# Optimization experiments

Hardware: AMD Instinct MI355X
Metric: run time of the kernel (lower is better)

Reference implementation:

```python
import jax, jax.numpy as jnp
import numpy as np

B, D, H, L = 65536, 512, 1024, 64
LOG2PI = float(np.log(2.0 * np.pi))


def setup_inputs() -> dict:
    key = jax.random.key(0)
    ks = jax.random.split(key, 16)
    s = jnp.float32(0.02)

    def w(k, shape):
        return jax.random.normal(k, shape, dtype=jnp.float32) * s

    return {
        "x": jax.random.normal(ks[0], (B, D), dtype=jnp.float32),
        "eps": jax.random.normal(ks[1], (B, L), dtype=jnp.float32),
        # encoder params (Linear stored as [in, out] for x @ W + b)
        "W_enc_h": w(ks[2], (D, H)), "b_enc_h": jnp.zeros((H,), jnp.float32),
        "W_enc_mu": w(ks[3], (H, L)), "b_enc_mu": jnp.zeros((L,), jnp.float32),
        "W_enc_lv": w(ks[4], (H, L)), "b_enc_lv": jnp.zeros((L,), jnp.float32),
        # decoder params
        "W_dec_h": w(ks[5], (L, H)), "b_dec_h": jnp.zeros((H,), jnp.float32),
        "W_dec_mu": w(ks[6], (H, D)), "b_dec_mu": jnp.zeros((D,), jnp.float32),
        "W_dec_lv": w(ks[7], (H, D)), "b_dec_lv": jnp.zeros((D,), jnp.float32),
    }


def reference(x, eps, W_enc_h, b_enc_h, W_enc_mu, b_enc_mu, W_enc_lv, b_enc_lv,
              W_dec_h, b_dec_h, W_dec_mu, b_dec_mu, W_dec_lv, b_dec_lv):
    beta = jnp.float32(1.0)
    # encoder
    h = jnp.tanh(x @ W_enc_h + b_enc_h)                      # [B, H]
    mu_z = h @ W_enc_mu + b_enc_mu                           # [B, L]
    lv_z = h @ W_enc_lv + b_enc_lv                           # [B, L]
    # reparameterised sample
    z = mu_z + jnp.exp(0.5 * lv_z) * eps                     # [B, L]
    # decoder
    hd = jnp.tanh(z @ W_dec_h + b_dec_h)                     # [B, H]
    mu_x = jax.nn.softmax(hd @ W_dec_mu + b_dec_mu, axis=-1) # [B, D]
    lv_x = hd @ W_dec_lv + b_dec_lv                          # [B, D]
    # KL(q(z|x) || N(0, I))
    kl = -0.5 * jnp.sum(1.0 + lv_z - mu_z ** 2 - jnp.exp(lv_z), axis=-1)  # [B]
    # diagonal Gaussian log-likelihood (closed form of MultivariateNormal
    # with diag_embed(exp(ln_var)) covariance)
    ln_pxz = -0.5 * jnp.sum(lv_x + (x - mu_x) ** 2 * jnp.exp(-lv_x) + LOG2PI, axis=-1)  # [B]
    return jnp.mean(ln_pxz - beta * kl)
```

## Files before the change

kernel.cpp:

```cpp
#include <hip/hip_runtime.h>

typedef unsigned char u8;
typedef unsigned short u16;
typedef unsigned int u32;
typedef long i64;
typedef __attribute__((ext_vector_type(2))) long long2v;
typedef __attribute__((ext_vector_type(4))) float floatx4;

#define LOG2PI_F 1.8378770664093453f

__device__ __forceinline__ u16 f2bf(float f) {
  union { float f; u32 i; } c; c.f = f;
  u32 i = c.i;
  u32 r = (i + 0x7fffu + ((i >> 16) & 1u)) >> 16;
  return (u16)r;
}
__device__ __forceinline__ float bf2f(u16 u) {
  union { u32 i; float f; } c; c.i = ((u32)u) << 16; return c.f;
}
__device__ __forceinline__ u8 f2fp8(float f) {
  int p = __builtin_amdgcn_cvt_pk_fp8_f32(f, f, 0, false);
  return (u8)(p & 0xff);
}
__device__ __forceinline__ u32 pk4fp8(float a, float b, float c, float d) {
  int lo = __builtin_amdgcn_cvt_pk_fp8_f32(a, b, 0, false);
  int v  = __builtin_amdgcn_cvt_pk_fp8_f32(c, d, lo, true);
  return (u32)v;
}
__device__ __forceinline__ float fast_tanh(float x) {
  float xc = fminf(fmaxf(x, -10.f), 10.f);
  float t = __expf(2.f * xc);
  return (t - 1.f) * __builtin_amdgcn_rcpf(t + 1.f);
}
__device__ __forceinline__ void llds16(const void* g, void* l) {
  __builtin_amdgcn_global_load_lds(
      (const __attribute__((address_space(1))) u32*)g,
      (__attribute__((address_space(3))) u32*)l, 16, 0, 0);
}
__device__ __forceinline__ u32 permk(u32 k) {
  u32 g = k & ~63u, o = (k >> 3) & 7u, r = k & 7u;
  u32 po = ((o & 3u) << 1) | (o >> 2);
  return g | (po << 3) | r;
}

#define INV_4096  2.44140625e-4f
#define INV_16384 6.103515625e-5f

__global__ void pack_xb(const float* __restrict__ in, u32* __restrict__ out, int n4) {
  int i = blockIdx.x * 256 + threadIdx.x;
  if (i >= n4) return;
  const float4 v = ((const float4*)in)[i];
  int row = i >> 7;
  int k = (i & 127) << 2;
  int kp = permk(k);
  out[(row << 7) + (kp >> 2)] = pk4fp8(v.x * 16.f, v.y * 16.f, v.z * 16.f, v.w * 16.f);
}

__global__ void pack_wt(const float* __restrict__ W, u8* __restrict__ Wt, int K, int N) {
  int idx = blockIdx.x * 256 + threadIdx.x;
  if (idx >= K * N) return;
  int k = idx / N, n = idx - k * N;
  Wt[(size_t)n * K + permk(k)] = f2fp8(W[idx] * 256.f);
}

__global__ void pack_wt2(const float* __restrict__ W1, const float* __restrict__ W2,
                         u8* __restrict__ Wt, int K, int N1, int N2) {
  int idx = blockIdx.x * 256 + threadIdx.x;
  if (idx >= (N1 + N2) * K) return;
  int n = idx / K, k = idx - n * K;
  float v = (n < N1) ? W1[(size_t)k * N1 + n] : W2[(size_t)k * N2 + (n - N1)];
  Wt[(size_t)n * K + permk(k)] = f2fp8(v * 256.f);
}

__global__ void catf(const float* __restrict__ a, const float* __restrict__ b,
                     float* __restrict__ o, int n1, int n2) {
  int i = blockIdx.x * 256 + threadIdx.x;
  if (i < n1) o[i] = a[i];
  else if (i < n1 + n2) o[i] = b[i - n1];
}

__global__ __launch_bounds__(256) void gemm_bt0(
    const u8* __restrict__ A, const u8* __restrict__ Bt,
    const float* __restrict__ bias, u8* __restrict__ C,
    float inv, float outs, int M, int N, int K) {
  __shared__ __align__(16) u8 smem[16384];
  u8* As = smem;
  u8* Bs = smem + 8192;
  const int t = threadIdx.x;
  const int wave = t >> 6, lane = t & 63;
  const int quad = lane >> 4, l16 = lane & 15;
  const int bm = blockIdx.y * 128, bn = blockIdx.x * 128;
  const int wm = (wave >> 1) * 64, wn = (wave & 1) * 64;

  floatx4 acc[4][4];
#pragma unroll
  for (int i = 0; i < 4; ++i)
#pragma unroll
    for (int j = 0; j < 4; ++j) acc[i][j] = (floatx4){0.f, 0.f, 0.f, 0.f};

  for (int kt = 0; kt < K; kt += 64) {
#pragma unroll
    for (int i = 0; i < 2; ++i) {
      int c = i * 256 + t;
      int r = c >> 2, kcS = c & 3;
      int kc = kcS ^ ((r >> 1) & 3);
      llds16(A + (size_t)(bm + r) * K + kt + kc * 16, &As[c * 16]);
      llds16(Bt + (size_t)(bn + r) * K + kt + kc * 16, &Bs[c * 16]);
    }
    __builtin_amdgcn_s_waitcnt(0);
    __syncthreads();

    long2v a2[4], b2[4];
#pragma unroll
    for (int mi = 0; mi < 4; ++mi) {
      int m = wm + mi * 16 + l16;
      a2[mi] = *(const long2v*)&As[(4 * m + (quad ^ ((m >> 1) & 3))) * 16];
    }
#pragma unroll
    for (int ni = 0; ni < 4; ++ni) {
      int n = wn + ni * 16 + l16;
      b2[ni] = *(const long2v*)&Bs[(4 * n + (quad ^ ((n >> 1) & 3))) * 16];
    }
#pragma unroll
    for (int h = 0; h < 2; ++h)
#pragma unroll
      for (int mi = 0; mi < 4; ++mi)
#pragma unroll
        for (int ni = 0; ni < 4; ++ni)
          acc[mi][ni] = __builtin_amdgcn_mfma_f32_16x16x32_fp8_fp8(
              a2[mi][h], b2[ni][h], acc[mi][ni], 0, 0, 0);
    __syncthreads();
  }

#pragma unroll
  for (int ni = 0; ni < 4; ++ni) {
    int col = wn + ni * 16 + l16;
    float bv = bias[bn + col];
    u32 pc = permk((u32)col);
#pragma unroll
    for (int mi = 0; mi < 4; ++mi) {
#pragma unroll
      for (int r = 0; r < 4; ++r) {
        int row = wm + mi * 16 + quad * 4 + r;
        float v = acc[mi][ni][r] * inv + bv;
        smem[row * 128 + pc] = f2fp8(fast_tanh(v) * outs);
      }
    }
  }
  __syncthreads();
#pragma unroll
  for (int j = 0; j < 4; ++j) {
    int u = j * 256 + t;
    int row = u >> 3, c16 = u & 7;
    *(long2v*)(C + (size_t)(bm + row) * N + bn + c16 * 16) =
        *(const long2v*)&smem[row * 128 + c16 * 16];
  }
}

template <int EPI>
__global__ __launch_bounds__(512, 2) void gemm256(
    const u8* __restrict__ A, const u8* __restrict__ Bt,
    const float* __restrict__ bias, void* __restrict__ Cv,
    float inv, float outs, int M, int N, int K) {
  __shared__ __align__(16) u8 lds[4][2][256 * 64];
  const int t = threadIdx.x;
  const int wave = t >> 6, lane = t & 63;
  const int quad = lane >> 4, l16 = lane & 15;
  const int nbx = N >> 8;
  const int nwg = nbx * (M >> 8);
  int raw = blockIdx.x + nbx * blockIdx.y;
  int wgid = ((nwg & 7) == 0) ? ((raw & 7) * (nwg >> 3) + (raw >> 3)) : raw;
  const int bm = (wgid / nbx) << 8, bn = (wgid % nbx) << 8;
  const int wm = (wave >> 2) * 128, wn = (wave & 3) * 64;
  const int nt = K >> 6;

  auto stage = [&](int ti) {
    const int b = ti & 3;
    const int kt = ti << 6;
#pragma unroll
    for (int i = 0; i < 2; ++i) {
      int c = i * 512 + t;
      int r = c >> 2, kcS = c & 3;
      int kc = kcS ^ ((r >> 1) & 3);
      llds16(A + (size_t)(bm + r) * K + kt + kc * 16, &lds[b][0][c * 16]);
    }
#pragma unroll
    for (int i = 0; i < 2; ++i) {
      int c = i * 512 + t;
      int r = c >> 2, kcS = c & 3;
      int kc = kcS ^ ((r >> 1) & 3);
      llds16(Bt + (size_t)(bn + r) * K + kt + kc * 16, &lds[b][1][c * 16]);
    }
  };

  int offA[8], offB[4];
#pragma unroll
  for (int mi = 0; mi < 8; ++mi) {
    int m = wm + mi * 16 + l16;
    offA[mi] = (4 * m + (quad ^ ((m >> 1) & 3))) * 16;
  }
#pragma unroll
  for (int ni = 0; ni < 4; ++ni) {
    int n = wn + ni * 16 + l16;
    offB[ni] = (4 * n + (quad ^ ((n >> 1) & 3))) * 16;
  }

  floatx4 acc[8][4];
#pragma unroll
  for (int i = 0; i < 8; ++i)
#pragma unroll
    for (int j = 0; j < 4; ++j) acc[i][j] = (floatx4){0.f, 0.f, 0.f, 0.f};

  long2v a2[8], b2[4], b3[4];

  stage(0);
  stage(1);
  asm volatile("s_waitcnt vmcnt(4)" ::: "memory");
  __builtin_amdgcn_s_barrier();
  asm volatile("" ::: "memory");
  {
    const u8* bA = &lds[0][0][0];
    const u8* bB = &lds[0][1][0];
#pragma unroll
    for (int ni = 0; ni < 4; ++ni) b2[ni] = *(const long2v*)(bB + offB[ni]);
#pragma unroll
    for (int mi = 0; mi < 8; ++mi) a2[mi] = *(const long2v*)(bA + offA[mi]);
  }

#define GBODY(TI, BCUR, BNXT) {                                               \
    const int ti_ = (TI);                                                     \
    if (ti_ + 2 < nt) {                                                       \
      stage(ti_ + 2);                                                         \
      asm volatile("s_waitcnt vmcnt(4)" ::: "memory");                        \
    } else {                                                                  \
      asm volatile("s_waitcnt vmcnt(0)" ::: "memory");                        \
    }                                                                         \
    __builtin_amdgcn_s_barrier();                                             \
    asm volatile("" ::: "memory");                                            \
    const u8* bA_ = &lds[(ti_ + 1) & 3][0][0];                                \
    const u8* bB_ = &lds[(ti_ + 1) & 3][1][0];                                \
    _Pragma("unroll")                                                         \
    for (int ni = 0; ni < 4; ++ni) BNXT[ni] = *(const long2v*)(bB_ + offB[ni]);\
    __builtin_amdgcn_s_setprio(1);                                            \
    _Pragma("unroll")                                                         \
    for (int mi = 0; mi < 8; ++mi) {                                          \
      _Pragma("unroll")                                                       \
      for (int h = 0; h < 2; ++h)                                             \
        _Pragma("unroll")                                                     \
        for (int ni = 0; ni < 4; ++ni)                                        \
          acc[mi][ni] = __builtin_amdgcn_mfma_f32_16x16x32_fp8_fp8(           \
              a2[mi][h], BCUR[ni][h], acc[mi][ni], 0, 0, 0);                  \
      a2[mi] = *(const long2v*)(bA_ + offA[mi]);                              \
    }                                                                         \
    __builtin_amdgcn_s_setprio(0);                                            \
  }

  int ti = 0;
  for (; ti + 2 < nt; ti += 2) {
    GBODY(ti, b2, b3);
    GBODY(ti + 1, b3, b2);
  }
  GBODY(ti, b2, b3);
#undef GBODY
  __builtin_amdgcn_s_setprio(1);
#pragma unroll
  for (int mi = 0; mi < 8; ++mi)
#pragma unroll
    for (int h = 0; h < 2; ++h)
#pragma unroll
      for (int ni = 0; ni < 4; ++ni)
        acc[mi][ni] = __builtin_amdgcn_mfma_f32_16x16x32_fp8_fp8(
            a2[mi][h], b3[ni][h], acc[mi][ni], 0, 0, 0);
  __builtin_amdgcn_s_setprio(0);

  __syncthreads();
  u8* eb = &lds[0][0][0];
  if (EPI == 0) {
#pragma unroll
    for (int ni = 0; ni < 4; ++ni) {
      int col = wn + ni * 16 + l16;
      float bv = bias[bn + col];
      u32 pc = permk((u32)col);
#pragma unroll
      for (int mi = 0; mi < 8; ++mi) {
#pragma unroll
        for (int r = 0; r < 4; ++r) {
          int row = wm + mi * 16 + quad * 4 + r;
          float v = acc[mi][ni][r] * inv + bv;
          eb[row * 256 + pc] = f2fp8(fast_tanh(v) * outs);
        }
      }
    }
    __syncthreads();
#pragma unroll
    for (int j = 0; j < 8; ++j) {
      int u = j * 512 + t;
      int row = u >> 4, c16 = u & 15;
      *(long2v*)((u8*)Cv + (size_t)(bm + row) * N + bn + c16 * 16) =
          *(const long2v*)&eb[row * 256 + c16 * 16];
    }
  } else {
    u16* ebw = (u16*)eb;
#pragma unroll
    for (int ni = 0; ni < 4; ++ni) {
      int col = wn + ni * 16 + l16;
      float bv = bias[bn + col];
#pragma unroll
      for (int mi = 0; mi < 8; ++mi) {
#pragma unroll
        for (int r = 0; r < 4; ++r) {
          int row = wm + mi * 16 + quad * 4 + r;
          float v = acc[mi][ni][r] * inv + bv;
          ebw[row * 256 + col] = f2bf(v);
        }
      }
    }
    __syncthreads();
#pragma unroll
    for (int j = 0; j < 16; ++j) {
      int u = j * 512 + t;
      int row = u >> 5, c16 = u & 31;
      *(long2v*)((u16*)Cv + (size_t)(bm + row) * N + bn + c16 * 8) =
          *(const long2v*)&ebw[row * 256 + c16 * 8];
    }
  }
}

__global__ __launch_bounds__(256) void gemm_z(
    const u8* __restrict__ A, const u8* __restrict__ Bt,
    const float* __restrict__ bias, const float* __restrict__ eps,
    u8* __restrict__ z, float* __restrict__ accp, int M, int K) {
  __shared__ __align__(16) u8 As[128 * 64];
  __shared__ __align__(16) u8 Bs[128 * 64];
  __shared__ float sexp[128 * 64];
  const int t = threadIdx.x;
  const int wave = t >> 6, lane = t & 63;
  const int quad = lane >> 4, l16 = lane & 15;
  const int bm = blockIdx.y * 128;
  const int wm = (wave >> 1) * 64, wn = (wave & 1) * 64;

  floatx4 acc[4][4];
#pragma unroll
  for (int i = 0; i < 4; ++i)
#pragma unroll
    for (int j = 0; j < 4; ++j) acc[i][j] = (floatx4){0.f, 0.f, 0.f, 0.f};

  for (int kt = 0; kt < K; kt += 64) {
#pragma unroll
    for (int i = 0; i < 2; ++i) {
      int c = i * 256 + t;
      int r = c >> 2, kcS = c & 3;
      int kc = kcS ^ ((r >> 1) & 3);
      llds16(A + (size_t)(bm + r) * K + kt + kc * 16, &As[c * 16]);
      llds16(Bt + (size_t)r * K + kt + kc * 16, &Bs[c * 16]);
    }
    __builtin_amdgcn_s_waitcnt(0);
    __syncthreads();

    long2v a2[4], b2[4];
#pragma unroll
    for (int mi = 0; mi < 4; ++mi) {
      int m = wm + mi * 16 + l16;
      a2[mi] = *(const long2v*)&As[(4 * m + (quad ^ ((m >> 1) & 3))) * 16];
    }
#pragma unroll
    for (int ni = 0; ni < 4; ++ni) {
      int n = wn + ni * 16 + l16;
      b2[ni] = *(const long2v*)&Bs[(4 * n + (quad ^ ((n >> 1) & 3))) * 16];
    }
#pragma unroll
    for (int h = 0; h < 2; ++h)
#pragma unroll
      for (int mi = 0; mi < 4; ++mi)
#pragma unroll
        for (int ni = 0; ni < 4; ++ni)
          acc[mi][ni] = __builtin_amdgcn_mfma_f32_16x16x32_fp8_fp8(
              a2[mi][h], b2[ni][h], acc[mi][ni], 0, 0, 0);
    __syncthreads();
  }

  const bool is_lv = (wave & 1);
  float kl = 0.f;
#pragma unroll
  for (int ni = 0; ni < 4; ++ni) {
    int col = wn + ni * 16 + l16;
    float bv = bias[col];
#pragma unroll
    for (int mi = 0; mi < 4; ++mi) {
#pragma unroll
      for (int r = 0; r < 4; ++r) {
        int row = wm + mi * 16 + quad * 4 + r;
        float v = acc[mi][ni][r] * INV_16384 + bv;
        if (is_lv) {
          kl += 1.0f + v - __expf(v);
          sexp[row * 64 + (col - 64)] = __expf(0.5f * v);
        } else {
          kl -= v * v;
        }
      }
    }
  }
  __syncthreads();
  if (!is_lv) {
#pragma unroll
    for (int ni = 0; ni < 4; ++ni) {
      int col = wn + ni * 16 + l16;
      float bv = bias[col];
#pragma unroll
      for (int mi = 0; mi < 4; ++mi) {
#pragma unroll
        for (int r = 0; r < 4; ++r) {
          int row = wm + mi * 16 + quad * 4 + r;
          float mu = acc[mi][ni][r] * INV_16384 + bv;
          size_t grow = (size_t)(bm + row);
          float ep = eps[grow * 64 + col];
          z[grow * 64 + permk(col)] = f2fp8((mu + sexp[row * 64 + col] * ep) * 16.f);
        }
      }
    }
  }
  kl *= 0.5f;
  for (int off = 32; off > 0; off >>= 1) kl += __shfl_xor(kl, off, 64);
  __shared__ float s4[4];
  if (lane == 0) s4[wave] = kl;
  __syncthreads();
  if (t == 0) atomicAdd(accp, s4[0] + s4[1] + s4[2] + s4[3]);
}

__global__ __launch_bounds__(256) void lik_kernel(
    const u16* __restrict__ loglv, const float* __restrict__ x,
    float* __restrict__ acc) {
  typedef __attribute__((ext_vector_type(8))) short short8;
  const int wave = threadIdx.x >> 6, lane = threadIdx.x & 63;
  float wacc = 0.f;
  for (int rr = 0; rr < 8; ++rr) {
    int row = blockIdx.x * 32 + wave * 8 + rr;
    const u16* Lr = loglv + (size_t)row * 1024;
    short8 lg8 = ((const short8*)Lr)[lane];
    float lg[8];
#pragma unroll
    for (int j = 0; j < 8; ++j) lg[j] = bf2f((u16)lg8[j]);
    float mx = lg[0];
#pragma unroll
    for (int j = 1; j < 8; ++j) mx = fmaxf(mx, lg[j]);
    for (int off = 32; off > 0; off >>= 1) mx = fmaxf(mx, __shfl_xor(mx, off, 64));
    float e[8], s = 0.f;
#pragma unroll
    for (int j = 0; j < 8; ++j) { e[j] = __expf(lg[j] - mx); s += e[j]; }
    for (int off = 32; off > 0; off >>= 1) s += __shfl_xor(s, off, 64);
    float inv_s = 1.0f / s;
    short8 lv8 = ((const short8*)Lr)[64 + lane];
    const float* xr = x + (size_t)row * 512 + lane * 8;
    float4 x0 = *(const float4*)xr, x1 = *(const float4*)(xr + 4);
    float xs[8] = {x0.x, x0.y, x0.z, x0.w, x1.x, x1.y, x1.z, x1.w};
    float T = 0.f;
#pragma unroll
    for (int j = 0; j < 8; ++j) {
      float lv = bf2f((u16)lv8[j]);
      float d = xs[j] - e[j] * inv_s;
      T += lv + d * d * __expf(-lv) + LOG2PI_F;
    }
    for (int off = 32; off > 0; off >>= 1) T += __shfl_xor(T, off, 64);
    if (lane == 0) wacc += -0.5f * T;
  }
  __shared__ float s4[4];
  if (lane == 0) s4[wave] = wacc;
  __syncthreads();
  if (threadIdx.x == 0) atomicAdd(acc, s4[0] + s4[1] + s4[2] + s4[3]);
}

__global__ void fin_kernel(const float* __restrict__ acc, float* __restrict__ out) {
  out[0] = acc[0] * (1.0f / 65536.0f);
}

extern "C" void kernel_launch(void* const* d_in, const int* in_sizes, int n_in,
                              void* d_out, int out_size, void* d_ws, size_t ws_size,
                              hipStream_t stream) {
  const int B = 65536, D = 512, H = 1024, L = 64;
  const float* x       = (const float*)d_in[0];
  const float* eps     = (const float*)d_in[1];
  const float* W_enc_h = (const float*)d_in[2];
  const float* b_enc_h = (const float*)d_in[3];
  const float* W_enc_mu= (const float*)d_in[4];
  const float* b_enc_mu= (const float*)d_in[5];
  const float* W_enc_lv= (const float*)d_in[6];
  const float* b_enc_lv= (const float*)d_in[7];
  const float* W_dec_h = (const float*)d_in[8];
  const float* b_dec_h = (const float*)d_in[9];
  const float* W_dec_mu= (const float*)d_in[10];
  const float* b_dec_mu= (const float*)d_in[11];
  const float* W_dec_lv= (const float*)d_in[12];
  const float* b_dec_lv= (const float*)d_in[13];

  char* ws = (char*)d_ws;
  u8*   Wt_eh  = (u8*)(ws + 0);
  u8*   Wt_z   = (u8*)(ws + 524288);
  u8*   Wt_dh  = (u8*)(ws + 655360);
  u8*   Wt_dx  = (u8*)(ws + 720896);
  float* bh    = (float*)(ws + 2097152);
  float* bz    = (float*)(ws + 2101248);
  float* bdh   = (float*)(ws + 2105344);
  float* bdx   = (float*)(ws + 2109440);
  float* acc   = (float*)(ws + 2113536);
  u8*   hbuf   = (u8*)(ws + 4194304);
  u8*   xb     = (u8*)(ws + 71303168);
  u8*   zbuf   = (u8*)(ws + 104857600);
  u16*  loglv  = (u16*)(ws + 109051904);

  hipMemsetAsync(acc, 0, 256, stream);

  pack_xb<<<(B * D / 4 + 255) / 256, 256, 0, stream>>>(x, (u32*)xb, B * D / 4);
  pack_wt<<<(D * H + 255) / 256, 256, 0, stream>>>(W_enc_h, Wt_eh, D, H);
  pack_wt2<<<(H * 2 * L + 255) / 256, 256, 0, stream>>>(W_enc_mu, W_enc_lv, Wt_z, H, L, L);
  pack_wt<<<(L * H + 255) / 256, 256, 0, stream>>>(W_dec_h, Wt_dh, L, H);
  pack_wt2<<<(H * 2 * D + 255) / 256, 256, 0, stream>>>(W_dec_mu, W_dec_lv, Wt_dx, H, D, D);
  catf<<<(H + 255) / 256, 256, 0, stream>>>(b_enc_h, b_enc_h, bh, H, 0);
  catf<<<(2 * L + 255) / 256, 256, 0, stream>>>(b_enc_mu, b_enc_lv, bz, L, L);
  catf<<<(H + 255) / 256, 256, 0, stream>>>(b_dec_h, b_dec_h, bdh, H, 0);
  catf<<<(2 * D + 255) / 256, 256, 0, stream>>>(b_dec_mu, b_dec_lv, bdx, D, D);

  gemm256<0><<<dim3(H / 256, B / 256), 512, 0, stream>>>(
      xb, Wt_eh, bh, hbuf, INV_4096, 64.f, B, H, D);
  gemm_z<<<dim3(1, B / 128), 256, 0, stream>>>(hbuf, Wt_z, bz, eps, zbuf, acc, B, H);
  gemm_bt0<<<dim3(H / 128, B / 128), 256, 0, stream>>>(
      zbuf, Wt_dh, bdh, hbuf, INV_4096, 64.f, B, H, L);
  gemm256<2><<<dim3(1024 / 256, B / 256), 512, 0, stream>>>(
      hbuf, Wt_dx, bdx, loglv, INV_16384, 0.f, B, 1024, H);
  lik_kernel<<<B / 32, 256, 0, stream>>>(loglv, x, acc);
  fin_kernel<<<1, 1, 0, stream>>>(acc, (float*)d_out);
}
```

Measured before the change: 551.2 us.

## Restructure GEMM mainloop to stage K-tile pairs with fewer barriers

Replaces the per-tile prefetch loop (one stage and one barrier per 64-wide K tile, two tiles in flight) with a pair-based schedule. It fills all four LDS buffers up front, then issues two tile loads at a time after each pair of compute clusters, using one barrier per tile instead of one per stage. The goal is to cut barrier and waitcnt overhead and let more tiles be in flight. In exchange it waits on vmcnt(0) more coarsely, which may expose load latency. It also assumes nt is even and at least 4, or the prologue stages out of range.

After: 865.1 us. 56.9% more time.

```diff
diff --git a/kernel.cpp b/kernel.cpp
--- a/kernel.cpp
+++ b/kernel.cpp
@@ -173,6 +173,7 @@
   const int bm = (wgid / nbx) << 8, bn = (wgid % nbx) << 8;
   const int wm = (wave >> 2) * 128, wn = (wave & 3) * 64;
   const int nt = K >> 6;
+  const int npair = nt >> 1;
 
   auto stage = [&](int ti) {
     const int b = ti & 3;
@@ -213,34 +214,7 @@
 
   long2v a2[8], b2[4], b3[4];
 
-  stage(0);
-  stage(1);
-  asm volatile("s_waitcnt vmcnt(4)" ::: "memory");
-  __builtin_amdgcn_s_barrier();
-  asm volatile("" ::: "memory");
-  {
-    const u8* bA = &lds[0][0][0];
-    const u8* bB = &lds[0][1][0];
-#pragma unroll
-    for (int ni = 0; ni < 4; ++ni) b2[ni] = *(const long2v*)(bB + offB[ni]);
-#pragma unroll
-    for (int mi = 0; mi < 8; ++mi) a2[mi] = *(const long2v*)(bA + offA[mi]);
-  }
-
-#define GBODY(TI, BCUR, BNXT) {                                               \
-    const int ti_ = (TI);                                                     \
-    if (ti_ + 2 < nt) {                                                       \
-      stage(ti_ + 2);                                                         \
-      asm volatile("s_waitcnt vmcnt(4)" ::: "memory");                        \
-    } else {                                                                  \
-      asm volatile("s_waitcnt vmcnt(0)" ::: "memory");                        \
-    }                                                                         \
-    __builtin_amdgcn_s_barrier();                                             \
-    asm volatile("" ::: "memory");                                            \
-    const u8* bA_ = &lds[(ti_ + 1) & 3][0][0];                                \
-    const u8* bB_ = &lds[(ti_ + 1) & 3][1][0];                                \
-    _Pragma("unroll")                                                         \
-    for (int ni = 0; ni < 4; ++ni) BNXT[ni] = *(const long2v*)(bB_ + offB[ni]);\
+#define CLUSTER_R(BREG, bA_) {                                                \
     __builtin_amdgcn_s_setprio(1);                                            \
     _Pragma("unroll")                                                         \
     for (int mi = 0; mi < 8; ++mi) {                                          \
@@ -249,29 +223,65 @@
         _Pragma("unroll")                                                     \
         for (int ni = 0; ni < 4; ++ni)                                        \
           acc[mi][ni] = __builtin_amdgcn_mfma_f32_16x16x32_fp8_fp8(           \
-              a2[mi][h], BCUR[ni][h], acc[mi][ni], 0, 0, 0);                  \
-      a2[mi] = *(const long2v*)(bA_ + offA[mi]);                              \
+              a2[mi][h], BREG[ni][h], acc[mi][ni], 0, 0, 0);                  \
+      a2[mi] = *(const long2v*)((bA_) + offA[mi]);                            \
     }                                                                         \
     __builtin_amdgcn_s_setprio(0);                                            \
   }
-
-  int ti = 0;
-  for (; ti + 2 < nt; ti += 2) {
-    GBODY(ti, b2, b3);
-    GBODY(ti + 1, b3, b2);
-  }
-  GBODY(ti, b2, b3);
-#undef GBODY
-  __builtin_amdgcn_s_setprio(1);
-#pragma unroll
-  for (int mi = 0; mi < 8; ++mi)
-#pragma unroll
-    for (int h = 0; h < 2; ++h)
-#pragma unroll
-      for (int ni = 0; ni < 4; ++ni)
-        acc[mi][ni] = __builtin_amdgcn_mfma_f32_16x16x32_fp8_fp8(
-            a2[mi][h], b3[ni][h], acc[mi][ni], 0, 0, 0);
-  __builtin_amdgcn_s_setprio(0);
+#define CLUSTER_N(BREG) {                                                     \
+    __builtin_amdgcn_s_setprio(1);                                            \
+    _Pragma("unroll")                                                         \
+    for (int mi = 0; mi < 8; ++mi)                                            \
+      _Pragma("unroll")                                                       \
+      for (int h = 0; h < 2; ++h)                                             \
+        _Pragma("unroll")                                                     \
+        for (int ni = 0; ni < 4; ++ni)                                        \
+          acc[mi][ni] = __builtin_amdgcn_mfma_f32_16x16x32_fp8_fp8(           \
+              a2[mi][h], BREG[ni][h], acc[mi][ni], 0, 0, 0);                  \
+    __builtin_amdgcn_s_setprio(0);                                            \
+  }
+
+  stage(0); stage(1); stage(2); stage(3);
+  asm volatile("s_waitcnt vmcnt(8)" ::: "memory");
+  __builtin_amdgcn_s_barrier();
+  asm volatile("" ::: "memory");
+  {
+    const u8* bA = &lds[0][0][0];
+    const u8* bB = &lds[0][1][0];
+#pragma unroll
+    for (int ni = 0; ni < 4; ++ni) b2[ni] = *(const long2v*)(bB + offB[ni]);
+#pragma unroll
+    for (int mi = 0; mi < 8; ++mi) a2[mi] = *(const long2v*)(bA + offA[mi]);
+  }
+
+  for (int p = 0; p < npair; ++p) {
+    const int t1i = 2 * p + 1;
+    const u8* sA1 = &lds[t1i & 3][0][0];
+    const u8* sB1 = &lds[t1i & 3][1][0];
+#pragma unroll
+    for (int ni = 0; ni < 4; ++ni) b3[ni] = *(const long2v*)(sB1 + offB[ni]);
+    CLUSTER_R(b2, sA1);
+    if (p + 1 < npair) {
+      asm volatile("s_waitcnt vmcnt(0)" ::: "memory");
+      __builtin_amdgcn_s_barrier();
+      asm volatile("" ::: "memory");
+      const int t2i = 2 * p + 2;
+      const u8* sA2 = &lds[t2i & 3][0][0];
+      const u8* sB2 = &lds[t2i & 3][1][0];
+#pragma unroll
+      for (int ni = 0; ni < 4; ++ni) b2[ni] = *(const long2v*)(sB2 + offB[ni]);
+      CLUSTER_R(b3, sA2);
+      asm volatile("s_waitcnt lgkmcnt(0)" ::: "memory");
+      __builtin_amdgcn_sched_barrier(0);
+      __builtin_amdgcn_s_barrier();
+      asm volatile("" ::: "memory");
+      if (p + 2 < npair) { stage(2 * p + 4); stage(2 * p + 5); }
+    } else {
+      CLUSTER_N(b3);
+    }
+  }
+#undef CLUSTER_R
+#undef CLUSTER_N
 
   __syncthreads();
   u8* eb = &lds[0][0][0];
```
